# Performance work log

Hardware: AMD Instinct MI355X
Metric: run time of the kernel (lower is better)

Reference implementation:

```python
import jax, jax.numpy as jnp
import numpy as np

N_NODES = 100000
N_EDGES = 1600000
NFEAT = 256
NHID = 64
NHEADS = 8
NCLASS = 97
ALPHA = 0.2  # leaky relu slope
EPS = 1e-16  # guard against isolated rows (pyGAT divides by e_rowsum directly)


def _sp_gat_layer(x, Wk, ak, src, dst, n_nodes, alpha, concat):
    """One SpGraphAttentionLayer (eval mode, dropout off).
    x: [N, f_in], Wk: [f_in, f_out], ak: [2*f_out].
    edge e_ij = exp(-leakyrelu(a . [h_i || h_j])), out[i] = sum_j e_ij h_j / sum_j e_ij.
    """
    h = x @ Wk                          # [N, f_out]
    f_out = Wk.shape[1]
    s_src = h @ ak[:f_out]              # [N] = a1 . h_i
    s_dst = h @ ak[f_out:]              # [N] = a2 . h_j
    e = jnp.exp(-jax.nn.leaky_relu(s_src[src] + s_dst[dst], negative_slope=alpha))  # [E]
    rowsum = jax.ops.segment_sum(e, src, num_segments=n_nodes)                       # [N]
    num = jax.ops.segment_sum(e[:, None] * h[dst], src, num_segments=n_nodes)        # [N, f_out]
    h_prime = num / (rowsum[:, None] + EPS)
    return jax.nn.elu(h_prime) if concat else h_prime


def setup_inputs() -> dict:
    key = jax.random.key(0)
    ks = jax.random.split(key, 6)
    gain = 1.414  # xavier gain used by pyGAT
    features = jax.random.normal(ks[0], (N_NODES, NFEAT), dtype=jnp.float32)
    edge_index = jax.random.randint(ks[1], (2, N_EDGES), 0, N_NODES, dtype=jnp.int64)
    W = jax.random.normal(ks[2], (NHEADS, NFEAT, NHID), dtype=jnp.float32) * (gain * np.sqrt(2.0 / (NFEAT + NHID)))
    a = jax.random.normal(ks[3], (NHEADS, 2 * NHID), dtype=jnp.float32) * (gain * np.sqrt(2.0 / (1 + 2 * NHID)))
    W_out = jax.random.normal(ks[4], (NHEADS * NHID, NCLASS), dtype=jnp.float32) * (gain * np.sqrt(2.0 / (NHEADS * NHID + NCLASS)))
    a_out = jax.random.normal(ks[5], (2 * NCLASS,), dtype=jnp.float32) * (gain * np.sqrt(2.0 / (1 + 2 * NCLASS)))
    return {"features": features, "W": W, "a": a, "W_out": W_out, "a_out": a_out, "edge_index": edge_index}


def reference(features, W, a, W_out, a_out, edge_index):
    src, dst = edge_index[0], edge_index[1]
    n = features.shape[0]
    # multi-head hidden layer, concat heads (loop over small fixed head count to bound memory)
    heads = [
        _sp_gat_layer(features, W[k], a[k], src, dst, n, ALPHA, concat=True)
        for k in range(W.shape[0])
    ]
    x = jnp.concatenate(heads, axis=1)  # [N, nheads*nhid]
    # output attention layer (concat=False), then elu + log_softmax as in SpGAT.forward
    x = _sp_gat_layer(x, W_out, a_out, src, dst, n, ALPHA, concat=False)
    return jax.nn.log_softmax(jax.nn.elu(x), axis=1)
```

## Files before the change

kernel.cpp:

```cpp
#include <hip/hip_runtime.h>
#include <hip/hip_bf16.h>
#include <stdint.h>

typedef __attribute__((ext_vector_type(8))) short short8;
typedef __attribute__((ext_vector_type(4))) float floatx4;
typedef uint32_t u32;

#define N_NODES 100000
#define N_EDGES 1600000
#define ALPHA_SLOPE 0.2f
#define EPS_F 1e-16f

static __device__ __forceinline__ float bf2f(ushort h) {
    u32 u = ((u32)h) << 16;
    return __builtin_bit_cast(float, u);
}
static __device__ __forceinline__ ushort f2bf(float f) {
    u32 u = __builtin_bit_cast(u32, f);
    u32 r = (u + 0x7fffu + ((u >> 16) & 1u)) >> 16;
    return (ushort)r;
}

__global__ __launch_bounds__(256) void conv_feat(
    const float* __restrict__ in, ushort* __restrict__ out, int n4)
{
    int i = blockIdx.x * 256 + threadIdx.x;
    if (i < n4) {
        float4 v = ((const float4*)in)[i];
        ushort4 o;
        o.x = f2bf(v.x); o.y = f2bf(v.y); o.z = f2bf(v.z); o.w = f2bf(v.w);
        ((ushort4*)out)[i] = o;
    }
}

__global__ __launch_bounds__(256) void pretranspose(
    const float* __restrict__ W, const float* __restrict__ Wout,
    ushort* __restrict__ Bp1, ushort* __restrict__ Bp2)
{
    int idx = blockIdx.x * 256 + threadIdx.x;
    if (idx < 256 * 512) {
        int k = idx >> 9, n = idx & 511;
        int head = n >> 6, c = n & 63;
        Bp1[((size_t)(k >> 3) * 512 + n) * 8 + (k & 7)] = f2bf(W[head * 16384 + k * 64 + c]);
    }
    if (idx < 512 * 128) {
        int k = idx >> 7, n = idx & 127;
        ushort v = (n < 97) ? f2bf(Wout[k * 97 + n]) : (ushort)0;
        Bp2[((size_t)(k >> 3) * 128 + n) * 8 + (k & 7)] = v;
    }
}

__global__ __launch_bounds__(256) void gemm_mfma(
    const ushort* __restrict__ A, const ushort* __restrict__ Bp,
    ushort* __restrict__ C, int M, int K, int NP)
{
    __shared__ __align__(16) ushort Ald[4 * 128 * 8];
    const int tid = threadIdx.x;
    const int lane = tid & 63;
    const int wave = tid >> 6;
    const int wr = wave >> 1, wc = wave & 1;
    const int row0 = blockIdx.x * 128;
    const int col0 = blockIdx.y * 128;
    const int quad = lane >> 4;
    const int l16 = lane & 15;

    floatx4 acc[4][4] = {};

    for (int k0 = 0; k0 < K; k0 += 32) {
        __syncthreads();
#pragma unroll
        for (int i = 0; i < 2; ++i) {
            int q = i * 256 + tid;
            int r = q >> 2, kq = q & 3;
            int row = row0 + r;
            if (row >= M) row = M - 1;
            const uint4* src = (const uint4*)(A + (size_t)row * K + k0 + kq * 8);
            *(uint4*)(&Ald[((kq * 128 + r) * 8)]) = *src;
        }
        __syncthreads();

        short8 bfrag[4];
        int kqg = (k0 >> 3) + quad;
#pragma unroll
        for (int nt = 0; nt < 4; ++nt) {
            int col = col0 + wc * 64 + nt * 16 + l16;
            bfrag[nt] = *(const short8*)(Bp + ((size_t)kqg * NP + col) * 8);
        }
#pragma unroll
        for (int mt = 0; mt < 4; ++mt) {
            int r = wr * 64 + mt * 16 + l16;
            short8 afrag = *(const short8*)(&Ald[(quad * 128 + r) * 8]);
#pragma unroll
            for (int nt = 0; nt < 4; ++nt) {
                acc[mt][nt] = __builtin_amdgcn_mfma_f32_16x16x32_bf16(afrag, bfrag[nt], acc[mt][nt], 0, 0, 0);
            }
        }
    }

#pragma unroll
    for (int mt = 0; mt < 4; ++mt) {
#pragma unroll
        for (int rr = 0; rr < 4; ++rr) {
            int row = row0 + wr * 64 + mt * 16 + quad * 4 + rr;
            if (row < M) {
#pragma unroll
                for (int nt = 0; nt < 4; ++nt) {
                    int col = col0 + wc * 64 + nt * 16 + l16;
                    C[(size_t)row * NP + col] = f2bf(acc[mt][nt][rr]);
                }
            }
        }
    }
}

__global__ __launch_bounds__(256) void sk1(
    const ushort* __restrict__ h_all, const float* __restrict__ a,
    float* __restrict__ ssrc, float* __restrict__ sdst, int N)
{
    int w = blockIdx.x * 4 + (threadIdx.x >> 6);
    int i = w >> 3, k = w & 7, l = threadIdx.x & 63;
    if (i >= N) return;
    float v = bf2f(h_all[(size_t)i * 512 + k * 64 + l]);
    float s1 = v * a[k * 128 + l];
    float s2 = v * a[k * 128 + 64 + l];
#pragma unroll
    for (int o = 32; o; o >>= 1) { s1 += __shfl_xor(s1, o); s2 += __shfl_xor(s2, o); }
    if (l == 0) { ssrc[i * 8 + k] = s1; sdst[i * 8 + k] = s2; }
}

__global__ __launch_bounds__(256) void hist(const int* __restrict__ ei, int* __restrict__ cnt, int E) {
    int e = blockIdx.x * 256 + threadIdx.x;
    if (e < E) atomicAdd(&cnt[ei[e]], 1);
}

__global__ __launch_bounds__(256) void scan_partial(const int* __restrict__ cnt, int* __restrict__ bsum, int N) {
    int idx = blockIdx.x * 256 + threadIdx.x;
    int v = (idx < N) ? cnt[idx] : 0;
#pragma unroll
    for (int o = 32; o; o >>= 1) v += __shfl_xor(v, o);
    __shared__ int ws[4];
    if ((threadIdx.x & 63) == 0) ws[threadIdx.x >> 6] = v;
    __syncthreads();
    if (threadIdx.x == 0) bsum[blockIdx.x] = ws[0] + ws[1] + ws[2] + ws[3];
}

__global__ __launch_bounds__(512) void scan_block(int* __restrict__ bsum, int nb) {
    __shared__ int s[512];
    int t = threadIdx.x;
    int v = (t < nb) ? bsum[t] : 0;
    s[t] = v;
    __syncthreads();
    for (int o = 1; o < 512; o <<= 1) {
        int u = (t >= o) ? s[t - o] : 0;
        __syncthreads();
        s[t] += u;
        __syncthreads();
    }
    if (t < nb) bsum[t] = s[t] - v;
}

__global__ __launch_bounds__(256) void scan_final(
    const int* __restrict__ cnt, const int* __restrict__ bsum,
    int* __restrict__ row_ptr, int N, int E)
{
    int b = blockIdx.x, t = threadIdx.x;
    int idx = b * 256 + t;
    int v = (idx < N) ? cnt[idx] : 0;
    __shared__ int s[256];
    s[t] = v;
    __syncthreads();
    for (int o = 1; o < 256; o <<= 1) {
        int u = (t >= o) ? s[t - o] : 0;
        __syncthreads();
        s[t] += u;
        __syncthreads();
    }
    if (idx < N) row_ptr[idx] = bsum[b] + s[t] - v;
    if (idx == 0) row_ptr[N] = E;
}

__global__ __launch_bounds__(256) void fill_csr(
    const int* __restrict__ ei, const int* __restrict__ row_ptr,
    int* __restrict__ cur, int* __restrict__ col_idx, int E)
{
    int e = blockIdx.x * 256 + threadIdx.x;
    if (e < E) {
        int s = ei[e];
        int d = ei[E + e];
        int p = atomicAdd(&cur[s], 1);
        col_idx[row_ptr[s] + p] = d;
    }
}

__global__ __launch_bounds__(256) void ea1(
    const int* __restrict__ row_ptr, const int* __restrict__ col_idx,
    const ushort* __restrict__ h_all, const float* __restrict__ ssrc,
    const float* __restrict__ sdst, ushort* __restrict__ x1)
{
    int i = blockIdx.x;
    int t = threadIdx.x;
    int hk = t >> 5;
    int start = row_ptr[i], end = row_ptr[i + 1];
    float si = ssrc[i * 8 + hk];
    float accx = 0.f, accy = 0.f, re = 0.f;
    __shared__ int dl[256];
    for (int j0 = start; j0 < end; j0 += 256) {
        int c = end - j0; if (c > 256) c = 256;
        __syncthreads();
        if (t < c) dl[t] = col_idx[j0 + t];
        __syncthreads();
        for (int jj = 0; jj < c; ++jj) {
            int d = dl[jj];
            float s = si + sdst[d * 8 + hk];
            float lr = s > 0.f ? s : ALPHA_SLOPE * s;
            float e = __expf(-lr);
            u32 hv = *(const u32*)(h_all + (size_t)d * 512 + 2 * t);
            accx = fmaf(e, bf2f((ushort)(hv & 0xffffu)), accx);
            accy = fmaf(e, bf2f((ushort)(hv >> 16)), accy);
            re += e;
        }
    }
    float inv = 1.f / (re + EPS_F);
    float px = accx * inv, py = accy * inv;
    px = px > 0.f ? px : expm1f(px);
    py = py > 0.f ? py : expm1f(py);
    u32 o = (u32)f2bf(px) | ((u32)f2bf(py) << 16);
    *(u32*)(x1 + (size_t)i * 512 + 2 * t) = o;
}

__global__ __launch_bounds__(256) void sk2(
    const ushort* __restrict__ h2p, const float* __restrict__ aout,
    float* __restrict__ s2src, float* __restrict__ s2dst, int N)
{
    int w = blockIdx.x * 4 + (threadIdx.x >> 6);
    if (w >= N) return;
    int l = threadIdx.x & 63;
    float s1 = 0.f, s2 = 0.f;
    for (int c = l; c < 97; c += 64) {
        float v = bf2f(h2p[(size_t)w * 128 + c]);
        s1 = fmaf(v, aout[c], s1);
        s2 = fmaf(v, aout[97 + c], s2);
    }
#pragma unroll
    for (int o = 32; o; o >>= 1) { s1 += __shfl_xor(s1, o); s2 += __shfl_xor(s2, o); }
    if (l == 0) { s2src[w] = s1; s2dst[w] = s2; }
}

__global__ __launch_bounds__(128) void ea2(
    const int* __restrict__ row_ptr, const int* __restrict__ col_idx,
    const ushort* __restrict__ h2p, const float* __restrict__ s2src,
    const float* __restrict__ s2dst, float* __restrict__ out)
{
    int i = blockIdx.x;
    int t = threadIdx.x;
    int start = row_ptr[i], end = row_ptr[i + 1];
    float si = s2src[i];
    float acc = 0.f, re = 0.f;
    __shared__ int dl[128];
    for (int j0 = start; j0 < end; j0 += 128) {
        int c = end - j0; if (c > 128) c = 128;
        __syncthreads();
        if (t < c) dl[t] = col_idx[j0 + t];
        __syncthreads();
        for (int jj = 0; jj < c; ++jj) {
            int d = dl[jj];
            float s = si + s2dst[d];
            float lr = s > 0.f ? s : ALPHA_SLOPE * s;
            float e = __expf(-lr);
            float hv = bf2f(h2p[(size_t)d * 128 + t]);
            acc = fmaf(e, hv, acc);
            re += e;
        }
    }
    float v = acc / (re + EPS_F);
    v = v > 0.f ? v : expm1f(v);
    bool valid = t < 97;
    float m = valid ? v : -1e30f;
#pragma unroll
    for (int o = 32; o; o >>= 1) m = fmaxf(m, __shfl_xor(m, o));
    __shared__ float smax[2], ssum[2];
    if ((t & 63) == 0) smax[t >> 6] = m;
    __syncthreads();
    m = fmaxf(smax[0], smax[1]);
    float ex = valid ? __expf(v - m) : 0.f;
#pragma unroll
    for (int o = 32; o; o >>= 1) ex += __shfl_xor(ex, o);
    if ((t & 63) == 0) ssum[t >> 6] = ex;
    __syncthreads();
    float tot = ssum[0] + ssum[1];
    if (valid) out[(size_t)i * 97 + t] = v - m - logf(tot);
}

extern "C" void kernel_launch(void* const* d_in, const int* in_sizes, int n_in,
                              void* d_out, int out_size, void* d_ws, size_t ws_size,
                              hipStream_t stream)
{
    const float* feat = (const float*)d_in[0];
    const float* W    = (const float*)d_in[1];
    const float* a    = (const float*)d_in[2];
    const float* Wout = (const float*)d_in[3];
    const float* aout = (const float*)d_in[4];
    const int*   ei   = (const int*)d_in[5];
    float* out = (float*)d_out;

    const int N = N_NODES, E = N_EDGES;
    const int NB = (N + 255) / 256;

    char* base = (char*)d_ws;
    ushort* h_all = (ushort*)(base);
    ushort* x1    = (ushort*)(base + 102400000);
    ushort* featb = (ushort*)(base + 204800000);
    ushort* h2p   = (ushort*)(base + 204800000);
    char* tail = base + 256000000;
    float* ssrc    = (float*)(tail + 0);
    float* sdst    = (float*)(tail + 3200000);
    float* s2src   = (float*)(tail + 6400000);
    float* s2dst   = (float*)(tail + 6800000);
    int*   row_ptr = (int*)(tail + 7200000);
    int*   cnt     = (int*)(tail + 7600128);
    int*   col_idx = (int*)(tail + 8000128);
    int*   bsum    = (int*)(tail + 14400128);
    ushort* Bp1    = (ushort*)(tail + 14401920);
    ushort* Bp2    = (ushort*)(tail + 14664064);

    hipMemsetAsync(cnt, 0, (size_t)N * 4, stream);
    conv_feat<<<(N * 256 / 4 + 255) / 256, 256, 0, stream>>>(feat, featb, N * 256 / 4);
    pretranspose<<<512, 256, 0, stream>>>(W, Wout, Bp1, Bp2);

    gemm_mfma<<<dim3(782, 4), 256, 0, stream>>>(featb, Bp1, h_all, N, 256, 512);
    sk1<<<(N * 8 + 3) / 4, 256, 0, stream>>>(h_all, a, ssrc, sdst, N);

    hist<<<(E + 255) / 256, 256, 0, stream>>>(ei, cnt, E);
    scan_partial<<<NB, 256, 0, stream>>>(cnt, bsum, N);
    scan_block<<<1, 512, 0, stream>>>(bsum, NB);
    scan_final<<<NB, 256, 0, stream>>>(cnt, bsum, row_ptr, N, E);
    hipMemsetAsync(cnt, 0, (size_t)N * 4, stream);
    fill_csr<<<(E + 255) / 256, 256, 0, stream>>>(ei, row_ptr, cnt, col_idx, E);

    ea1<<<N, 256, 0, stream>>>(row_ptr, col_idx, h_all, ssrc, sdst, x1);

    gemm_mfma<<<dim3(782, 1), 256, 0, stream>>>(x1, Bp2, h2p, N, 512, 128);
    sk2<<<(N + 3) / 4, 256, 0, stream>>>(h2p, aout, s2src, s2dst, N);
    ea2<<<N, 128, 0, stream>>>(row_ptr, col_idx, h2p, s2src, s2dst, out);
}
```

Before: 944.0 us.

## Precompute edge attention weights and switch aggregation to wave-per-row

Edge attention weights for both layers are now computed once per edge in separate passes (folded into the CSR fill for layer 1, and a new per-edge kernel for layer 2) and stored in CSR order. The aggregation kernels move from one block per node to one 64-lane wavefront per node, with each lane loading 8 (layer 1) or 2 (layer 2) bf16 features per neighbour. This removes the shared-memory staging, the block barriers and the repeated per-thread exp calls. The cost is extra edge-sized weight buffers (8 floats per edge for layer 1) that have to be written and read back, plus a source-row array.

```diff
diff --git a/kernel.cpp b/kernel.cpp
--- a/kernel.cpp
+++ b/kernel.cpp
@@ -181,51 +181,65 @@
 
 __global__ __launch_bounds__(256) void fill_csr(
     const int* __restrict__ ei, const int* __restrict__ row_ptr,
-    int* __restrict__ cur, int* __restrict__ col_idx, int E)
+    int* __restrict__ cur, int* __restrict__ col_idx, int* __restrict__ srow,
+    const float* __restrict__ ssrc, const float* __restrict__ sdst,
+    float* __restrict__ ew1, int E)
 {
     int e = blockIdx.x * 256 + threadIdx.x;
-    if (e < E) {
-        int s = ei[e];
-        int d = ei[E + e];
-        int p = atomicAdd(&cur[s], 1);
-        col_idx[row_ptr[s] + p] = d;
-    }
+    if (e >= E) return;
+    int s = ei[e];
+    int d = ei[E + e];
+    int p = atomicAdd(&cur[s], 1);
+    int slot = row_ptr[s] + p;
+    col_idx[slot] = d;
+    srow[slot] = s;
+    float4 as0 = *(const float4*)(ssrc + s * 8);
+    float4 as1 = *(const float4*)(ssrc + s * 8 + 4);
+    float4 ad0 = *(const float4*)(sdst + d * 8);
+    float4 ad1 = *(const float4*)(sdst + d * 8 + 4);
+    float sc[8] = { as0.x + ad0.x, as0.y + ad0.y, as0.z + ad0.z, as0.w + ad0.w,
+                    as1.x + ad1.x, as1.y + ad1.y, as1.z + ad1.z, as1.w + ad1.w };
+    float ev[8];
+#pragma unroll
+    for (int h = 0; h < 8; ++h) {
+        float v = sc[h];
+        float lr = v > 0.f ? v : ALPHA_SLOPE * v;
+        ev[h] = __expf(-lr);
+    }
+    float4* dst = (float4*)(ew1 + (size_t)slot * 8);
+    dst[0] = make_float4(ev[0], ev[1], ev[2], ev[3]);
+    dst[1] = make_float4(ev[4], ev[5], ev[6], ev[7]);
 }
 
 __global__ __launch_bounds__(256) void ea1(
     const int* __restrict__ row_ptr, const int* __restrict__ col_idx,
-    const ushort* __restrict__ h_all, const float* __restrict__ ssrc,
-    const float* __restrict__ sdst, ushort* __restrict__ x1)
-{
-    int i = blockIdx.x;
-    int t = threadIdx.x;
-    int hk = t >> 5;
-    int start = row_ptr[i], end = row_ptr[i + 1];
-    float si = ssrc[i * 8 + hk];
-    float accx = 0.f, accy = 0.f, re = 0.f;
-    __shared__ int dl[256];
-    for (int j0 = start; j0 < end; j0 += 256) {
-        int c = end - j0; if (c > 256) c = 256;
-        __syncthreads();
-        if (t < c) dl[t] = col_idx[j0 + t];
-        __syncthreads();
-        for (int jj = 0; jj < c; ++jj) {
-            int d = dl[jj];
-            float s = si + sdst[d * 8 + hk];
-            float lr = s > 0.f ? s : ALPHA_SLOPE * s;
-            float e = __expf(-lr);
-            u32 hv = *(const u32*)(h_all + (size_t)d * 512 + 2 * t);
-            accx = fmaf(e, bf2f((ushort)(hv & 0xffffu)), accx);
-            accy = fmaf(e, bf2f((ushort)(hv >> 16)), accy);
-            re += e;
-        }
+    const ushort* __restrict__ h_all, const float* __restrict__ ew1,
+    ushort* __restrict__ x1)
+{
+    int w = blockIdx.x * 4 + (threadIdx.x >> 6);
+    int l = threadIdx.x & 63;
+    int hl = l >> 3;
+    int start = row_ptr[w], end = row_ptr[w + 1];
+    float acc[8] = {};
+    float re = 0.f;
+    for (int j = start; j < end; ++j) {
+        int d = col_idx[j];
+        float e = ew1[(size_t)j * 8 + hl];
+        short8 hv = *(const short8*)(h_all + (size_t)d * 512 + l * 8);
+        re += e;
+#pragma unroll
+        for (int q = 0; q < 8; ++q)
+            acc[q] = fmaf(e, bf2f((ushort)hv[q]), acc[q]);
     }
     float inv = 1.f / (re + EPS_F);
-    float px = accx * inv, py = accy * inv;
-    px = px > 0.f ? px : expm1f(px);
-    py = py > 0.f ? py : expm1f(py);
-    u32 o = (u32)f2bf(px) | ((u32)f2bf(py) << 16);
-    *(u32*)(x1 + (size_t)i * 512 + 2 * t) = o;
+    short8 o;
+#pragma unroll
+    for (int q = 0; q < 8; ++q) {
+        float p = acc[q] * inv;
+        p = p > 0.f ? p : expm1f(p);
+        o[q] = (short)f2bf(p);
+    }
+    *(short8*)(x1 + (size_t)w * 512 + l * 8) = o;
 }
 
 __global__ __launch_bounds__(256) void sk2(
@@ -246,49 +260,51 @@
     if (l == 0) { s2src[w] = s1; s2dst[w] = s2; }
 }
 
-__global__ __launch_bounds__(128) void ea2(
+__global__ __launch_bounds__(256) void ew2k(
+    const int* __restrict__ srow, const int* __restrict__ col_idx,
+    const float* __restrict__ s2src, const float* __restrict__ s2dst,
+    float* __restrict__ ew2, int E)
+{
+    int j = blockIdx.x * 256 + threadIdx.x;
+    if (j < E) {
+        float s = s2src[srow[j]] + s2dst[col_idx[j]];
+        float lr = s > 0.f ? s : ALPHA_SLOPE * s;
+        ew2[j] = __expf(-lr);
+    }
+}
+
+__global__ __launch_bounds__(256) void ea2(
     const int* __restrict__ row_ptr, const int* __restrict__ col_idx,
-    const ushort* __restrict__ h2p, const float* __restrict__ s2src,
-    const float* __restrict__ s2dst, float* __restrict__ out)
-{
-    int i = blockIdx.x;
-    int t = threadIdx.x;
-    int start = row_ptr[i], end = row_ptr[i + 1];
-    float si = s2src[i];
-    float acc = 0.f, re = 0.f;
-    __shared__ int dl[128];
-    for (int j0 = start; j0 < end; j0 += 128) {
-        int c = end - j0; if (c > 128) c = 128;
-        __syncthreads();
-        if (t < c) dl[t] = col_idx[j0 + t];
-        __syncthreads();
-        for (int jj = 0; jj < c; ++jj) {
-            int d = dl[jj];
-            float s = si + s2dst[d];
-            float lr = s > 0.f ? s : ALPHA_SLOPE * s;
-            float e = __expf(-lr);
-            float hv = bf2f(h2p[(size_t)d * 128 + t]);
-            acc = fmaf(e, hv, acc);
-            re += e;
-        }
-    }
-    float v = acc / (re + EPS_F);
-    v = v > 0.f ? v : expm1f(v);
-    bool valid = t < 97;
-    float m = valid ? v : -1e30f;
+    const ushort* __restrict__ h2p, const float* __restrict__ ew2,
+    float* __restrict__ out)
+{
+    int w = blockIdx.x * 4 + (threadIdx.x >> 6);
+    int l = threadIdx.x & 63;
+    int start = row_ptr[w], end = row_ptr[w + 1];
+    float a0 = 0.f, a1 = 0.f, re = 0.f;
+    for (int j = start; j < end; ++j) {
+        int d = col_idx[j];
+        float e = ew2[j];
+        u32 hv = *(const u32*)(h2p + (size_t)d * 128 + 2 * l);
+        re += e;
+        a0 = fmaf(e, bf2f((ushort)(hv & 0xffffu)), a0);
+        a1 = fmaf(e, bf2f((ushort)(hv >> 16)), a1);
+    }
+    float inv = 1.f / (re + EPS_F);
+    float v0 = a0 * inv, v1 = a1 * inv;
+    v0 = v0 > 0.f ? v0 : expm1f(v0);
+    v1 = v1 > 0.f ? v1 : expm1f(v1);
+    int c0 = 2 * l, c1 = 2 * l + 1;
+    bool val0 = c0 < 97, val1 = c1 < 97;
+    float m = fmaxf(val0 ? v0 : -1e30f, val1 ? v1 : -1e30f);
 #pragma unroll
     for (int o = 32; o; o >>= 1) m = fmaxf(m, __shfl_xor(m, o));
-    __shared__ float smax[2], ssum[2];
-    if ((t & 63) == 0) smax[t >> 6] = m;
-    __syncthreads();
-    m = fmaxf(smax[0], smax[1]);
-    float ex = valid ? __expf(v - m) : 0.f;
+    float ex = (val0 ? __expf(v0 - m) : 0.f) + (val1 ? __expf(v1 - m) : 0.f);
 #pragma unroll
     for (int o = 32; o; o >>= 1) ex += __shfl_xor(ex, o);
-    if ((t & 63) == 0) ssum[t >> 6] = ex;
-    __syncthreads();
-    float tot = ssum[0] + ssum[1];
-    if (valid) out[(size_t)i * 97 + t] = v - m - logf(tot);
+    float lt = m + logf(ex);
+    if (val0) out[(size_t)w * 97 + c0] = v0 - lt;
+    if (val1) out[(size_t)w * 97 + c1] = v1 - lt;
 }
 
 extern "C" void kernel_launch(void* const* d_in, const int* in_sizes, int n_in,
@@ -310,6 +326,7 @@
     ushort* h_all = (ushort*)(base);
     ushort* x1    = (ushort*)(base + 102400000);
     ushort* featb = (ushort*)(base + 204800000);
+    float*  ew1   = (float*)(base + 204800000);
     ushort* h2p   = (ushort*)(base + 204800000);
     char* tail = base + 256000000;
     float* ssrc    = (float*)(tail + 0);
@@ -322,6 +339,8 @@
     int*   bsum    = (int*)(tail + 14400128);
     ushort* Bp1    = (ushort*)(tail + 14401920);
     ushort* Bp2    = (ushort*)(tail + 14664064);
+    int*   srow    = (int*)(tail + 14795136);
+    float* ew2     = (float*)(tail + 21195136);
 
     hipMemsetAsync(cnt, 0, (size_t)N * 4, stream);
     conv_feat<<<(N * 256 / 4 + 255) / 256, 256, 0, stream>>>(feat, featb, N * 256 / 4);
@@ -335,11 +354,12 @@
     scan_block<<<1, 512, 0, stream>>>(bsum, NB);
     scan_final<<<NB, 256, 0, stream>>>(cnt, bsum, row_ptr, N, E);
     hipMemsetAsync(cnt, 0, (size_t)N * 4, stream);
-    fill_csr<<<(E + 255) / 256, 256, 0, stream>>>(ei, row_ptr, cnt, col_idx, E);
-
-    ea1<<<N, 256, 0, stream>>>(row_ptr, col_idx, h_all, ssrc, sdst, x1);
+    fill_csr<<<(E + 255) / 256, 256, 0, stream>>>(ei, row_ptr, cnt, col_idx, srow, ssrc, sdst, ew1, E);
+
+    ea1<<<N / 4, 256, 0, stream>>>(row_ptr, col_idx, h_all, ew1, x1);
 
     gemm_mfma<<<dim3(782, 1), 256, 0, stream>>>(x1, Bp2, h2p, N, 512, 128);
     sk2<<<(N + 3) / 4, 256, 0, stream>>>(h2p, aout, s2src, s2dst, N);
-    ea2<<<N, 128, 0, stream>>>(row_ptr, col_idx, h2p, s2src, s2dst, out);
-}
+    ew2k<<<(E + 255) / 256, 256, 0, stream>>>(srow, col_idx, s2src, s2dst, ew2, E);
+    ea2<<<N / 4, 256, 0, stream>>>(row_ptr, col_idx, h2p, ew2, out);
+}
```

Measured after the change: 1.023 ms. 1.08x slower.
